# Kernel optimization log

Hardware: AMD Instinct MI355X
Metric: run time of the kernel (lower is better)

The kernel has to match this reference:

```python
import jax, jax.numpy as jnp
import numpy as np

N_NODES = 50000
N_EDGES = 800000
HID = 64
N_LAYERS = 3
N_GRAPHS = 64
NEG_SLOPE = 0.01  # nn.LeakyReLU default


def setup_inputs() -> dict:
    key = jax.random.key(0)
    ks = jax.random.split(key, 10)
    return {
        "x": jax.random.normal(ks[0], (N_NODES, HID), dtype=jnp.float32),
        "edge_attr": jax.random.normal(ks[1], (N_EDGES,), dtype=jnp.float32),
        "edge_w": jax.random.normal(ks[2], (N_LAYERS, 1, HID), dtype=jnp.float32) * 0.1,
        "edge_b": jax.random.normal(ks[3], (N_LAYERS, HID), dtype=jnp.float32) * 0.1,
        "node_w": jax.random.normal(ks[4], (N_LAYERS, 2 * HID, HID), dtype=jnp.float32) * 0.05,
        "node_b": jax.random.normal(ks[5], (N_LAYERS, HID), dtype=jnp.float32) * 0.1,
        "fc_w": jax.random.normal(ks[6], (HID, 1), dtype=jnp.float32) * 0.1,
        "fc_b": jax.random.normal(ks[7], (1,), dtype=jnp.float32) * 0.1,
        "edge_index": jax.random.randint(ks[8], (2, N_EDGES), 0, N_NODES, dtype=jnp.int32),
        "batch": jnp.sort(jax.random.randint(ks[9], (N_NODES,), 0, N_GRAPHS, dtype=jnp.int32)),
    }


def reference(x, edge_attr, edge_w, edge_b, node_w, node_b, fc_w, fc_b, edge_index, batch):
    src = edge_index[0]  # x_j gathered from source nodes
    dst = edge_index[1]  # aggregated into target nodes (aggr='add')
    ea = edge_attr.reshape(-1, 1)  # [E, 1]
    for l in range(N_LAYERS):
        edge_emb = ea @ edge_w[l] + edge_b[l]                       # [E, H] edge MLP
        msg = jnp.concatenate([x[src], edge_emb], axis=1)            # [E, 2H] message
        aggr = jax.ops.segment_sum(msg, dst, num_segments=N_NODES)   # [N, 2H] scatter-add
        x = jax.nn.relu(aggr @ node_w[l] + node_b[l])                # update: node MLP + ReLU
        x = jnp.where(x >= 0, x, NEG_SLOPE * x)                      # LeakyReLU (dropout=0)
    # global_mean_pool over batch assignment
    sums = jax.ops.segment_sum(x, batch, num_segments=N_GRAPHS)      # [G, H]
    counts = jax.ops.segment_sum(jnp.ones((x.shape[0], 1), x.dtype), batch, num_segments=N_GRAPHS)
    pooled = sums / jnp.maximum(counts, 1.0)
    return pooled @ fc_w + fc_b  # [G, 1]
```

## Files before the change

### kernel.cpp

```cpp
#include <hip/hip_runtime.h>

#define N_NODES 50000
#define N_EDGES 800000
#define HID 64
#define N_LAYERS 3
#define N_GRAPHS 64
#define MAXDEG 64
#define FIXS 4096.0f

typedef unsigned int u32;
typedef unsigned short ushort_t;
typedef short bf16x8 __attribute__((ext_vector_type(8)));
typedef float f32x4 __attribute__((ext_vector_type(4)));

__device__ __forceinline__ ushort_t f2bf(float f) {
    unsigned int u = __builtin_bit_cast(unsigned int, f);
    unsigned int r = u + 0x7fffu + ((u >> 16) & 1u);
    return (ushort_t)(r >> 16);
}
__device__ __forceinline__ float lo16(u32 u) { return __builtin_bit_cast(float, u << 16); }
__device__ __forceinline__ float hi16(u32 u) { return __builtin_bit_cast(float, u & 0xffff0000u); }

__global__ __launch_bounds__(256) void edge_cvt_uv_kernel(
        const int* __restrict__ src, const int* __restrict__ dst,
        const float* __restrict__ ea,
        int* __restrict__ cnt, u32* __restrict__ ell,
        const float* __restrict__ x_in, uint4* __restrict__ xbf0,
        const int* __restrict__ batch, int* __restrict__ gstart,
        const float* __restrict__ edge_w, const float* __restrict__ edge_b,
        const float* __restrict__ node_w, float* __restrict__ uv,
        int edgeBlocks, int cvtBlocks, int gbBlocks) {
    int t = threadIdx.x;
    int b = (int)blockIdx.x;
    if (b < edgeBlocks) {
        int e = b * 256 + t;
        if (e >= N_EDGES) return;
        int d = dst[e];
        float fv = (ea[e] + 8.0f) * FIXS;
        fv = fminf(fmaxf(fv, 0.0f), 65535.0f);
        u32 fx = __float2uint_rn(fv);
        int pos = atomicAdd(&cnt[d], 1);
        if (pos < MAXDEG) ell[((size_t)d << 6) + pos] = (u32)src[e] | (fx << 16);
        return;
    }
    if (b < edgeBlocks + cvtBlocks) {
        int i = (b - edgeBlocks) * 256 + t;
        if (i < N_NODES * HID / 8) {
            const float4* p = (const float4*)(x_in + (size_t)i * 8);
            float4 a = p[0], c = p[1];
            uint4 o;
            o.x = (u32)f2bf(a.x) | ((u32)f2bf(a.y) << 16);
            o.y = (u32)f2bf(a.z) | ((u32)f2bf(a.w) << 16);
            o.z = (u32)f2bf(c.x) | ((u32)f2bf(c.y) << 16);
            o.w = (u32)f2bf(c.z) | ((u32)f2bf(c.w) << 16);
            xbf0[i] = o;
        }
        return;
    }
    if (b < edgeBlocks + cvtBlocks + gbBlocks) {
        int i = (b - edgeBlocks - cvtBlocks) * 256 + t;
        if (i >= N_NODES) return;
        int bi = batch[i];
        if (i == 0) {
            for (int g = 0; g <= bi; g++) gstart[g] = 0;
        } else {
            int bp = batch[i - 1];
            for (int g = bp + 1; g <= bi; g++) gstart[g] = i;
        }
        if (i == N_NODES - 1) {
            for (int g = bi + 1; g <= N_GRAPHS; g++) gstart[g] = N_NODES;
        }
        return;
    }
    if (t >= N_LAYERS * HID) return;
    int l = t >> 6, hp = t & 63;
    const float* w2 = node_w + l * 2 * HID * HID + HID * HID + hp;
    float u = 0.f, v = 0.f;
    for (int h = 0; h < HID; h++) {
        float w = w2[h * HID];
        u += edge_w[l * HID + h] * w;
        v += edge_b[l * HID + h] * w;
    }
    uv[l * 2 * HID + hp]       = u;
    uv[l * 2 * HID + HID + hp] = v;
}

__global__ __launch_bounds__(128) void agg_mfma_kernel(
        const ushort_t* __restrict__ xbf, const u32* __restrict__ ell,
        const int* __restrict__ cnt,
        const float* __restrict__ W1, const float* __restrict__ node_b_l,
        const float* __restrict__ uv_l, float* __restrict__ sattr,
        int layer0, ushort_t* __restrict__ out_bf, float* __restrict__ out_f32) {
    __shared__ float redA[64][9];
    __shared__ float redB[64][9];
    __shared__ u32   redS[64];
    int lane = threadIdx.x & 63;
    int half = threadIdx.x >> 6;
    int nodeBase = blockIdx.x * 16;
    int q = lane >> 4, n15 = lane & 15;

    int m = nodeBase + n15;
    int dg = cnt[m]; if (dg > MAXDEG) dg = MAXDEG;
    int mx = dg;
#pragma unroll
    for (int off = 1; off < 16; off <<= 1) {
        int o = __shfl_xor(mx, off);
        mx = o > mx ? o : mx;
    }

    const uint4* erow4 = (const uint4*)(ell + ((size_t)m << 6));
    const uint4* xrows = (const uint4*)xbf;
    float accA[8] = {0,0,0,0,0,0,0,0};
    float accB[8] = {0,0,0,0,0,0,0,0};
    u32 sfix = 0;
    int base = half * 4;
    uint4 e4 = {0, 0, 0, 0};
    if (base < mx) e4 = erow4[base >> 2];
    for (; base < mx; base += 8) {
        int nbase = base + 8;
        uint4 e4n = {0, 0, 0, 0};
        if (nbase < mx) e4n = erow4[nbase >> 2];
        u32 ee[4] = {e4.x, e4.y, e4.z, e4.w};
        uint4 lo[4], hi[4];
        float f[4];
#pragma unroll
        for (int k = 0; k < 4; k++) {
            bool v = (base + k) < dg;
            u32 e = ee[k];
            sfix += v ? (e >> 16) : 0u;
            int s = v ? (int)(e & 0xffffu) : 0;
            lo[k] = xrows[(size_t)s * 8 + q];
            hi[k] = xrows[(size_t)s * 8 + 4 + q];
            f[k] = v ? 1.0f : 0.0f;
        }
#pragma unroll
        for (int k = 0; k < 4; k++) {
            accA[0] += f[k] * lo16(lo[k].x); accA[1] += f[k] * hi16(lo[k].x);
            accA[2] += f[k] * lo16(lo[k].y); accA[3] += f[k] * hi16(lo[k].y);
            accA[4] += f[k] * lo16(lo[k].z); accA[5] += f[k] * hi16(lo[k].z);
            accA[6] += f[k] * lo16(lo[k].w); accA[7] += f[k] * hi16(lo[k].w);
            accB[0] += f[k] * lo16(hi[k].x); accB[1] += f[k] * hi16(hi[k].x);
            accB[2] += f[k] * lo16(hi[k].y); accB[3] += f[k] * hi16(hi[k].y);
            accB[4] += f[k] * lo16(hi[k].z); accB[5] += f[k] * hi16(hi[k].z);
            accB[6] += f[k] * lo16(hi[k].w); accB[7] += f[k] * hi16(hi[k].w);
        }
        e4 = e4n;
    }

    if (half == 1) {
#pragma unroll
        for (int j = 0; j < 8; j++) { redA[lane][j] = accA[j]; redB[lane][j] = accB[j]; }
        redS[lane] = sfix;
    }
    __syncthreads();
    if (half == 1) return;
#pragma unroll
    for (int j = 0; j < 8; j++) { accA[j] += redA[lane][j]; accB[j] += redB[lane][j]; }
    sfix += redS[lane];

    float satv;
    if (layer0) {
        satv = (float)(int)sfix * (1.0f / FIXS) - 8.0f * (float)dg;
        if (lane < 16) sattr[nodeBase + lane] = satv;
    } else {
        satv = sattr[m];
    }

    bf16x8 af0, af1;
#pragma unroll
    for (int j = 0; j < 8; j++) {
        af0[j] = (short)f2bf(accA[j]);
        af1[j] = (short)f2bf(accB[j]);
    }

    int q8 = q * 8;
    f32x4 c[4];
#pragma unroll
    for (int nt = 0; nt < 4; nt++) {
        bf16x8 b0, b1;
#pragma unroll
        for (int j = 0; j < 8; j++) {
            b0[j] = (short)f2bf(W1[(q8 + j) * HID + nt * 16 + n15]);
            b1[j] = (short)f2bf(W1[(32 + q8 + j) * HID + nt * 16 + n15]);
        }
        f32x4 z = {0.f, 0.f, 0.f, 0.f};
        c[nt] = __builtin_amdgcn_mfma_f32_16x16x32_bf16(af0, b0, z, 0, 0, 0);
        c[nt] = __builtin_amdgcn_mfma_f32_16x16x32_bf16(af1, b1, c[nt], 0, 0, 0);
    }

    float dgown = (float)dg;
    float sat[4], dgf[4];
#pragma unroll
    for (int r = 0; r < 4; r++) {
        int srcLane = q * 4 + r;
        sat[r] = __shfl(satv, srcLane);
        dgf[r] = __shfl(dgown, srcLane);
    }
#pragma unroll
    for (int nt = 0; nt < 4; nt++) {
        int col = nt * 16 + n15;
        float uc = uv_l[col], vc = uv_l[HID + col], bc = node_b_l[col];
#pragma unroll
        for (int r = 0; r < 4; r++) {
            int n = nodeBase + q * 4 + r;
            float val = c[nt][r] + sat[r] * uc + dgf[r] * vc + bc;
            val = val > 0.f ? val : 0.f;
            if (out_bf) out_bf[(size_t)n * HID + col] = f2bf(val);
            else        out_f32[(size_t)n * HID + col] = val;
        }
    }
}

__global__ __launch_bounds__(256) void pool_fc_kernel(
        const float* __restrict__ x, const int* __restrict__ gstart,
        const float* __restrict__ fc_w, const float* __restrict__ fc_b,
        float* __restrict__ out) {
    __shared__ float red[4][HID];
    int g = blockIdx.x;
    int lane = threadIdx.x & 63, w = threadIdx.x >> 6;
    int s = gstart[g], e = gstart[g + 1];
    float acc = 0.f;
    int r = s + w;
    for (; r + 12 < e; r += 16) {
        float a0 = x[(size_t)(r     ) * HID + lane];
        float a1 = x[(size_t)(r +  4) * HID + lane];
        float a2 = x[(size_t)(r +  8) * HID + lane];
        float a3 = x[(size_t)(r + 12) * HID + lane];
        acc += a0 + a1 + a2 + a3;
    }
    for (; r < e; r += 4) acc += x[(size_t)r * HID + lane];
    red[w][lane] = acc;
    __syncthreads();
    if (w != 0) return;
    acc = red[0][lane] + red[1][lane] + red[2][lane] + red[3][lane];
    float dot = acc * fc_w[lane];
    for (int off = 32; off > 0; off >>= 1) dot += __shfl_down(dot, off);
    if (lane == 0) {
        float cntf = (float)(e - s);
        if (cntf < 1.f) cntf = 1.f;
        out[g] = dot / cntf + fc_b[0];
    }
}

extern "C" void kernel_launch(void* const* d_in, const int* in_sizes, int n_in,
                              void* d_out, int out_size, void* d_ws, size_t ws_size,
                              hipStream_t stream) {
    const float* x_in      = (const float*)d_in[0];
    const float* edge_attr = (const float*)d_in[1];
    const float* edge_w    = (const float*)d_in[2];
    const float* edge_b    = (const float*)d_in[3];
    const float* node_w    = (const float*)d_in[4];
    const float* node_b    = (const float*)d_in[5];
    const float* fc_w      = (const float*)d_in[6];
    const float* fc_b      = (const float*)d_in[7];
    const int*   edge_index= (const int*)d_in[8];
    const int*   batch     = (const int*)d_in[9];
    float* out = (float*)d_out;

    ushort_t* xbf0  = (ushort_t*)d_ws;
    ushort_t* xbf1  = xbf0 + (size_t)N_NODES * HID;
    float*    xA    = (float*)(xbf1 + (size_t)N_NODES * HID);
    u32*      ell   = (u32*)(xA + (size_t)N_NODES * HID);
    int*      cnt   = (int*)(ell + (size_t)N_NODES * MAXDEG);
    int*      gstart= cnt + N_NODES;
    float*    sattr = (float*)(gstart + N_GRAPHS + 1);
    float*    uv    = sattr + N_NODES;

    const int* src = edge_index;
    const int* dst = edge_index + N_EDGES;

    hipMemsetAsync(cnt, 0, (size_t)N_NODES * sizeof(int), stream);

    const int EB  = (N_EDGES + 255) / 256;
    const int CVT = (N_NODES * HID / 8 + 255) / 256;
    const int GB  = (N_NODES + 255) / 256;
    edge_cvt_uv_kernel<<<EB + CVT + GB + 1, 256, 0, stream>>>(
        src, dst, edge_attr, cnt, ell, x_in, (uint4*)xbf0, batch, gstart,
        edge_w, edge_b, node_w, uv, EB, CVT, GB);

    const int AGG_BLOCKS = N_NODES / 16;
    agg_mfma_kernel<<<AGG_BLOCKS, 128, 0, stream>>>(
        xbf0, ell, cnt, node_w, node_b, uv, sattr, 1, xbf1, nullptr);
    agg_mfma_kernel<<<AGG_BLOCKS, 128, 0, stream>>>(
        xbf1, ell, cnt, node_w + (size_t)2 * HID * HID, node_b + HID, uv + 2 * HID,
        sattr, 0, xbf0, nullptr);
    agg_mfma_kernel<<<AGG_BLOCKS, 128, 0, stream>>>(
        xbf0, ell, cnt, node_w + (size_t)4 * HID * HID, node_b + 2 * HID, uv + 4 * HID,
        sattr, 0, nullptr, xA);

    pool_fc_kernel<<<N_GRAPHS, 256, 0, stream>>>(xA, gstart, fc_w, fc_b, out);
}
```

Baseline: 219.3 us.

## Split neighbor gather across four waves and vectorize edge ELL build

```diff
diff --git a/kernel.cpp b/kernel.cpp
--- a/kernel.cpp
+++ b/kernel.cpp
@@ -33,14 +33,27 @@
     int t = threadIdx.x;
     int b = (int)blockIdx.x;
     if (b < edgeBlocks) {
-        int e = b * 256 + t;
-        if (e >= N_EDGES) return;
-        int d = dst[e];
-        float fv = (ea[e] + 8.0f) * FIXS;
-        fv = fminf(fmaxf(fv, 0.0f), 65535.0f);
-        u32 fx = __float2uint_rn(fv);
-        int pos = atomicAdd(&cnt[d], 1);
-        if (pos < MAXDEG) ell[((size_t)d << 6) + pos] = (u32)src[e] | (fx << 16);
+        int base = (b * 256 + t) * 4;
+        if (base >= N_EDGES) return;
+        int4   dv = *(const int4*)(dst + base);
+        int4   sv = *(const int4*)(src + base);
+        float4 av = *(const float4*)(ea + base);
+        int   dd[4] = {dv.x, dv.y, dv.z, dv.w};
+        int   ss[4] = {sv.x, sv.y, sv.z, sv.w};
+        float aa[4] = {av.x, av.y, av.z, av.w};
+        u32 fx[4];
+#pragma unroll
+        for (int k = 0; k < 4; k++) {
+            float fv = (aa[k] + 8.0f) * FIXS;
+            fv = fminf(fmaxf(fv, 0.0f), 65535.0f);
+            fx[k] = __float2uint_rn(fv);
+        }
+        int pos[4];
+#pragma unroll
+        for (int k = 0; k < 4; k++) pos[k] = atomicAdd(&cnt[dd[k]], 1);
+#pragma unroll
+        for (int k = 0; k < 4; k++)
+            if (pos[k] < MAXDEG) ell[((size_t)dd[k] << 6) + pos[k]] = (u32)ss[k] | (fx[k] << 16);
         return;
     }
     if (b < edgeBlocks + cvtBlocks) {
@@ -85,17 +98,17 @@
     uv[l * 2 * HID + HID + hp] = v;
 }
 
-__global__ __launch_bounds__(128) void agg_mfma_kernel(
+__global__ __launch_bounds__(256) void agg_mfma_kernel(
         const ushort_t* __restrict__ xbf, const u32* __restrict__ ell,
         const int* __restrict__ cnt,
         const float* __restrict__ W1, const float* __restrict__ node_b_l,
         const float* __restrict__ uv_l, float* __restrict__ sattr,
         int layer0, ushort_t* __restrict__ out_bf, float* __restrict__ out_f32) {
-    __shared__ float redA[64][9];
-    __shared__ float redB[64][9];
-    __shared__ u32   redS[64];
+    __shared__ float redA[3][64][9];
+    __shared__ float redB[3][64][9];
+    __shared__ u32   redS[3][64];
     int lane = threadIdx.x & 63;
-    int half = threadIdx.x >> 6;
+    int w = threadIdx.x >> 6;
     int nodeBase = blockIdx.x * 16;
     int q = lane >> 4, n15 = lane & 15;
 
@@ -113,11 +126,11 @@
     float accA[8] = {0,0,0,0,0,0,0,0};
     float accB[8] = {0,0,0,0,0,0,0,0};
     u32 sfix = 0;
-    int base = half * 4;
+    int base = w * 4;
     uint4 e4 = {0, 0, 0, 0};
     if (base < mx) e4 = erow4[base >> 2];
-    for (; base < mx; base += 8) {
-        int nbase = base + 8;
+    for (; base < mx; base += 16) {
+        int nbase = base + 16;
         uint4 e4n = {0, 0, 0, 0};
         if (nbase < mx) e4n = erow4[nbase >> 2];
         u32 ee[4] = {e4.x, e4.y, e4.z, e4.w};
@@ -147,16 +160,19 @@
         e4 = e4n;
     }
 
-    if (half == 1) {
-#pragma unroll
-        for (int j = 0; j < 8; j++) { redA[lane][j] = accA[j]; redB[lane][j] = accB[j]; }
-        redS[lane] = sfix;
+    if (w != 0) {
+#pragma unroll
+        for (int j = 0; j < 8; j++) { redA[w - 1][lane][j] = accA[j]; redB[w - 1][lane][j] = accB[j]; }
+        redS[w - 1][lane] = sfix;
     }
     __syncthreads();
-    if (half == 1) return;
-#pragma unroll
-    for (int j = 0; j < 8; j++) { accA[j] += redA[lane][j]; accB[j] += redB[lane][j]; }
-    sfix += redS[lane];
+    if (w != 0) return;
+#pragma unroll
+    for (int p = 0; p < 3; p++) {
+#pragma unroll
+        for (int j = 0; j < 8; j++) { accA[j] += redA[p][lane][j]; accB[j] += redB[p][lane][j]; }
+        sfix += redS[p][lane];
+    }
 
     float satv;
     if (layer0) {
@@ -271,7 +287,7 @@
 
     hipMemsetAsync(cnt, 0, (size_t)N_NODES * sizeof(int), stream);
 
-    const int EB  = (N_EDGES + 255) / 256;
+    const int EB  = (N_EDGES / 4 + 255) / 256;
     const int CVT = (N_NODES * HID / 8 + 255) / 256;
     const int GB  = (N_NODES + 255) / 256;
     edge_cvt_uv_kernel<<<EB + CVT + GB + 1, 256, 0, stream>>>(
@@ -279,12 +295,12 @@
         edge_w, edge_b, node_w, uv, EB, CVT, GB);
 
     const int AGG_BLOCKS = N_NODES / 16;
-    agg_mfma_kernel<<<AGG_BLOCKS, 128, 0, stream>>>(
+    agg_mfma_kernel<<<AGG_BLOCKS, 256, 0, stream>>>(
         xbf0, ell, cnt, node_w, node_b, uv, sattr, 1, xbf1, nullptr);
-    agg_mfma_kernel<<<AGG_BLOCKS, 128, 0, stream>>>(
+    agg_mfma_kernel<<<AGG_BLOCKS, 256, 0, stream>>>(
         xbf1, ell, cnt, node_w + (size_t)2 * HID * HID, node_b + HID, uv + 2 * HID,
         sattr, 0, xbf0, nullptr);
-    agg_mfma_kernel<<<AGG_BLOCKS, 128, 0, stream>>>(
+    agg_mfma_kernel<<<AGG_BLOCKS, 256, 0, stream>>>(
         xbf0, ell, cnt, node_w + (size_t)4 * HID * HID, node_b + 2 * HID, uv + 4 * HID,
         sattr, 0, nullptr, xA);
 
```

Result: slower. 223.7 us (+2.0%).
